# Kernel optimization log

Hardware: AMD Instinct MI355X
Metric: run time of the kernel (lower is better)

## Reference

```python
import jax, jax.numpy as jnp
import numpy as np

EMBED = 768
HEADS = 12
HEAD_DIM = EMBED // HEADS
HIDDEN = int(EMBED * 4.0)
EPS = 1e-5


def setup_inputs() -> dict:
    key = jax.random.key(0)
    ks = jax.random.split(key, 12)
    s = 0.02
    return {
        "x": jax.random.normal(ks[0], (8, 1024, EMBED), dtype=jnp.float32),
        # norm1 / norm2 (LayerNorm affine params)
        "g1": jnp.ones((EMBED,), jnp.float32),
        "b1": jnp.zeros((EMBED,), jnp.float32),
        "g2": jnp.ones((EMBED,), jnp.float32),
        "b2": jnp.zeros((EMBED,), jnp.float32),
        # attention weights (stored [in, out]; qkv_bias=False)
        "w_qkv": jax.random.normal(ks[1], (EMBED, 3 * EMBED), jnp.float32) * s,
        "w_proj": jax.random.normal(ks[2], (EMBED, EMBED), jnp.float32) * s,
        "b_proj": jnp.zeros((EMBED,), jnp.float32),
        # MLP weights
        "w_fc1": jax.random.normal(ks[3], (EMBED, HIDDEN), jnp.float32) * s,
        "b_fc1": jnp.zeros((HIDDEN,), jnp.float32),
        "w_fc2": jax.random.normal(ks[4], (HIDDEN, EMBED), jnp.float32) * s,
        "b_fc2": jnp.zeros((EMBED,), jnp.float32),
    }


def _layernorm(x, g, b):
    mu = jnp.mean(x, axis=-1, keepdims=True)
    var = jnp.var(x, axis=-1, keepdims=True)
    return (x - mu) * jax.lax.rsqrt(var + EPS) * g + b


def reference(x, g1, b1, g2, b2, w_qkv, w_proj, b_proj, w_fc1, b_fc1, w_fc2, b_fc2):
    B, N, C = x.shape
    scaling = HEAD_DIM ** (-0.5)

    # --- attention branch ---
    h = _layernorm(x, g1, b1)
    qkv = (h @ w_qkv).reshape(B, N, 3, HEADS, HEAD_DIM)
    q, k, v = qkv[:, :, 0], qkv[:, :, 1], qkv[:, :, 2]  # [B, N, H, D]
    attn = jnp.einsum("bnhd,bmhd->bhnm", q, k) * scaling  # full NxN scores
    attn = jax.nn.softmax(attn, axis=-1)
    out = jnp.einsum("bhnm,bmhd->bnhd", attn, v).reshape(B, N, C)
    out = out @ w_proj + b_proj
    x = x + out

    # --- MLP branch ---
    h = _layernorm(x, g2, b2)
    h = jax.nn.gelu(h @ w_fc1 + b_fc1, approximate=False)
    h = h @ w_fc2 + b_fc2
    return x + h
```

## Files before the change

kernel.cpp:

```cpp
#include <hip/hip_runtime.h>
#include <hip/hip_bf16.h>
#include <math.h>

#define EMBED 768
#define HEADS 12
#define HEAD_DIM 64
#define HIDDEN 3072
#define SEQ 1024
#define BATCH 8
#define TOKENS (SEQ*BATCH)

typedef unsigned short u16;
typedef __attribute__((ext_vector_type(8))) short bf16x8;
typedef __attribute__((ext_vector_type(4))) float floatx4;
typedef __attribute__((ext_vector_type(4))) u16 u16x4;
typedef __attribute__((ext_vector_type(2))) u16 u16x2;

__device__ __forceinline__ u16 f2bf(float f){
    union { float f; unsigned u; } v; v.f = f;
    unsigned r = v.u + 0x7fffu + ((v.u >> 16) & 1u);
    return (u16)(r >> 16);
}

__device__ __forceinline__ void gload16(const void* g, void* l){
    __builtin_amdgcn_global_load_lds((const __attribute__((address_space(1))) void*)g,
                                     (__attribute__((address_space(3))) void*)l, 16, 0, 0);
}

__device__ __forceinline__ float gelu_fast(float x){
    float t = 1.5957691216f * (x + 0.044715f * x * x * x);
    return x / (1.0f + __expf(-t));
}

__global__ void transpose_cast_all(const float* __restrict__ w0, const float* __restrict__ w1,
                                   const float* __restrict__ w2, const float* __restrict__ w3,
                                   u16* __restrict__ o0, u16* __restrict__ o1,
                                   u16* __restrict__ o2, u16* __restrict__ o3){
    int bb = blockIdx.x;
    const float* W; u16* Wt; int K, N, bx, by;
    if(bb < 1728)      { int l = bb;        W=w0; Wt=o0; K=768;  N=2304; bx=l%72; by=l/72; }
    else if(bb < 2304) { int l = bb-1728;   W=w1; Wt=o1; K=768;  N=768;  bx=l%24; by=l/24; }
    else if(bb < 4608) { int l = bb-2304;   W=w2; Wt=o2; K=768;  N=3072; bx=l%96; by=l/96; }
    else               { int l = bb-4608;   W=w3; Wt=o3; K=3072; N=768;  bx=l%24; by=l/24; }

    __shared__ float tile[32][33];
    int n0 = bx * 32, k0 = by * 32;
    int tx = threadIdx.x, ty = threadIdx.y;
    #pragma unroll
    for(int i=0;i<32;i+=8) tile[ty+i][tx] = W[(size_t)(k0+ty+i)*N + n0+tx];
    __syncthreads();
    int tid = ty*32 + tx;
    int kp = (tid & 15)*2, nn = tid >> 4;
    #pragma unroll
    for(int p=0;p<2;p++){
        int n = nn + p*16;
        u16x2 w2v;
        w2v.x = f2bf(tile[kp  ][n]);
        w2v.y = f2bf(tile[kp+1][n]);
        *(u16x2*)(Wt + (size_t)(n0+n)*K + k0 + kp) = w2v;
    }
}

__global__ __launch_bounds__(256) void ln_kernel(const float* __restrict__ x, const float* __restrict__ g,
                                                 const float* __restrict__ b, u16* __restrict__ out){
    int row  = blockIdx.x * 4 + (threadIdx.x >> 6);
    int lane = threadIdx.x & 63;
    const float4* xr = (const float4*)(x + (size_t)row * EMBED);
    float4 v[3];
    float s = 0.f;
    #pragma unroll
    for(int i=0;i<3;i++){
        v[i] = xr[i*64 + lane];
        s += v[i].x + v[i].y + v[i].z + v[i].w;
    }
    #pragma unroll
    for(int o=32;o>0;o>>=1) s += __shfl_xor(s, o);
    float mu = s * (1.0f/EMBED);
    float s2 = 0.f;
    #pragma unroll
    for(int i=0;i<3;i++){
        float dx = v[i].x-mu, dy = v[i].y-mu, dz = v[i].z-mu, dw = v[i].w-mu;
        s2 += dx*dx + dy*dy + dz*dz + dw*dw;
    }
    #pragma unroll
    for(int o=32;o>0;o>>=1) s2 += __shfl_xor(s2, o);
    float rstd = rsqrtf(s2*(1.0f/EMBED) + 1e-5f);
    u16* orow = out + (size_t)row * EMBED;
    const float4* g4 = (const float4*)g;
    const float4* b4 = (const float4*)b;
    #pragma unroll
    for(int i=0;i<3;i++){
        int c4 = i*64 + lane;
        float4 gv = g4[c4], bv = b4[c4];
        u16x4 pk;
        pk.x = f2bf((v[i].x-mu)*rstd*gv.x + bv.x);
        pk.y = f2bf((v[i].y-mu)*rstd*gv.y + bv.y);
        pk.z = f2bf((v[i].z-mu)*rstd*gv.z + bv.z);
        pk.w = f2bf((v[i].w-mu)*rstd*gv.w + bv.w);
        *(u16x4*)(orow + c4*4) = pk;
    }
}

template<int EPI, int BM>
__global__ __launch_bounds__(256) void gemm_bt(const u16* __restrict__ A, const u16* __restrict__ Bt,
        void* __restrict__ Cout, const float* __restrict__ bias, const float* __restrict__ res,
        u16* __restrict__ vt, int M, int N, int K, int ldc){
    constexpr int MF  = BM/32;
    constexpr int ASZ = BM*64;
    constexpr int BSZ = 128*64;
    __shared__ __align__(16) u16 As[2*ASZ];
    __shared__ __align__(16) u16 Bs[2*BSZ];
    int tid  = threadIdx.x;
    int wave = tid >> 6, lane = tid & 63;
    int quad = lane >> 4, lm = lane & 15;
    int m0 = blockIdx.y * BM, n0 = blockIdx.x * 128;
    int wm = (wave & 1) * (BM/2);
    int wn = (wave >> 1) * 64;

    floatx4 acc[MF][4];
    #pragma unroll
    for(int i=0;i<MF;i++)
        #pragma unroll
        for(int j=0;j<4;j++) acc[i][j] = (floatx4){0.f,0.f,0.f,0.f};

    int srow = tid >> 3;
    int scol = ((tid & 7) ^ (srow & 7)) * 8;
    const u16* aP[MF];
    const u16* bP[4];
    #pragma unroll
    for(int p=0;p<MF;p++) aP[p] = A  + (size_t)(m0 + p*32 + srow) * K + scol;
    #pragma unroll
    for(int p=0;p<4;p++)  bP[p] = Bt + (size_t)(n0 + p*32 + srow) * K + scol;

    #pragma unroll
    for(int p=0;p<MF;p++) gload16(aP[p], As + p*2048 + tid*8);
    #pragma unroll
    for(int p=0;p<4;p++)  gload16(bP[p], Bs + p*2048 + tid*8);
    __syncthreads();

    int cur = 0;
    for(int k0=0; k0<K; k0+=64){
        int nxt = cur ^ 1;
        if(k0 + 64 < K){
            #pragma unroll
            for(int p=0;p<MF;p++) gload16(aP[p] + k0 + 64, As + nxt*ASZ + p*2048 + tid*8);
            #pragma unroll
            for(int p=0;p<4;p++)  gload16(bP[p] + k0 + 64, Bs + nxt*BSZ + p*2048 + tid*8);
        }
        const u16* Asb = As + cur*ASZ;
        const u16* Bsb = Bs + cur*BSZ;
        #pragma unroll
        for(int ks=0;ks<2;ks++){
            int slotoff = (((ks*4+quad) ^ (lm&7)) << 3);
            bf16x8 af[MF], bfr[4];
            #pragma unroll
            for(int i=0;i<MF;i++)
                af[i]  = *(const bf16x8*)(Asb + (wm + i*16 + lm)*64 + slotoff);
            #pragma unroll
            for(int i=0;i<4;i++)
                bfr[i] = *(const bf16x8*)(Bsb + (wn + i*16 + lm)*64 + slotoff);
            #pragma unroll
            for(int mf=0;mf<MF;mf++)
                #pragma unroll
                for(int nf=0;nf<4;nf++)
                    acc[mf][nf] = __builtin_amdgcn_mfma_f32_16x16x32_bf16(af[mf], bfr[nf], acc[mf][nf], 0, 0, 0);
        }
        if(k0 + 64 < K) __syncthreads();
        cur = nxt;
    }

    if(EPI == 3 && n0 >= 1536){
        #pragma unroll
        for(int nf=0;nf<4;nf++){
            int col = n0 + wn + nf*16 + lm;
            int hh = (col - 1536) >> 6;
            int d  = col & 63;
            #pragma unroll
            for(int mf=0;mf<MF;mf++){
                int row0 = m0 + wm + mf*16 + quad*4;
                int bb  = row0 >> 10;
                int key = row0 & 1023;
                u16x4 pk;
                #pragma unroll
                for(int r=0;r<4;r++) pk[r] = f2bf(acc[mf][nf][r]);
                *(u16x4*)(vt + ((size_t)(bb*HEADS+hh)*64 + d)*SEQ + key) = pk;
            }
        }
        return;
    }

    #pragma unroll
    for(int nf=0;nf<4;nf++){
        int col = n0 + wn + nf*16 + lm;
        float bv = bias ? bias[col] : 0.f;
        #pragma unroll
        for(int mf=0;mf<MF;mf++){
            int row0 = m0 + wm + mf*16 + quad*4;
            #pragma unroll
            for(int r=0;r<4;r++){
                float v = acc[mf][nf][r] + bv;
                size_t idx = (size_t)(row0 + r) * ldc + col;
                if(EPI == 1){
                    v = gelu_fast(v);
                    ((u16*)Cout)[idx] = f2bf(v);
                } else if(EPI == 2){
                    ((float*)Cout)[idx] = v + res[idx];
                } else {
                    ((u16*)Cout)[idx] = f2bf(v);
                }
            }
        }
    }
}

__global__ __launch_bounds__(256) void attn_kernel(const u16* __restrict__ qk, const u16* __restrict__ vt,
                                                   u16* __restrict__ out){
    int qt = blockIdx.x, h = blockIdx.y, b = blockIdx.z;
    int tid = threadIdx.x;
    int wave = tid >> 6, lane = tid & 63;
    int quad = lane >> 4, lm = lane & 15;

    __shared__ __align__(16) u16 Ks[2*64*64];
    __shared__ __align__(16) u16 Vs[2*64*64];
    __shared__ __align__(16) u16 P[4*32*64];

    const u16* qbase = qk + (size_t)b * SEQ * 1536;
    const u16* vbase = vt + (size_t)(b*HEADS + h) * 64 * SEQ;
    u16* Pw = P + wave*2048;

    int q0 = qt*128 + wave*32;
    bf16x8 qf[2][2];
    #pragma unroll
    for(int qi=0;qi<2;qi++){
        const u16* qp = qbase + (size_t)(q0 + qi*16 + lm)*1536 + h*64;
        qf[qi][0] = *(const bf16x8*)(qp + quad*8);
        qf[qi][1] = *(const bf16x8*)(qp + 32 + quad*8);
    }

    float l_i[2] = {0.f, 0.f};
    floatx4 o_acc[2][4];
    #pragma unroll
    for(int qi=0;qi<2;qi++)
        #pragma unroll
        for(int nf=0;nf<4;nf++) o_acc[qi][nf] = (floatx4){0.f,0.f,0.f,0.f};

    int sr = lane >> 3;
    int sp = lane & 7;
    const float C = 0.18033688011112186f;

    auto stage = [&](int kt, int buf){
        #pragma unroll
        for(int i=0;i<2;i++){
            int rr = wave*16 + i*8 + sr;
            int sw = (sp ^ (rr & 7)) * 8;
            gload16(qbase + (size_t)(kt*64 + rr)*1536 + 768 + h*64 + sw,
                    Ks + buf*4096 + (wave*16 + i*8)*64 + lane*8);
            gload16(vbase + (size_t)rr*SEQ + kt*64 + sw,
                    Vs + buf*4096 + (wave*16 + i*8)*64 + lane*8);
        }
    };

    stage(0, 0);
    __syncthreads();

    int cur = 0;
    for(int kt=0; kt<16; kt++){
        if(kt < 15) stage(kt+1, cur^1);
        const u16* Ksb = Ks + cur*4096;
        const u16* Vsb = Vs + cur*4096;

        floatx4 s[4][2];
        #pragma unroll
        for(int kf=0;kf<4;kf++){
            int krow = kf*16 + lm;
            bf16x8 k0 = *(const bf16x8*)(Ksb + krow*64 + ((quad     ^ (lm&7))*8));
            bf16x8 k1 = *(const bf16x8*)(Ksb + krow*64 + (((4+quad) ^ (lm&7))*8));
            #pragma unroll
            for(int qi=0;qi<2;qi++){
                floatx4 t = (floatx4){0.f,0.f,0.f,0.f};
                t = __builtin_amdgcn_mfma_f32_16x16x32_bf16(k0, qf[qi][0], t, 0, 0, 0);
                t = __builtin_amdgcn_mfma_f32_16x16x32_bf16(k1, qf[qi][1], t, 0, 0, 0);
                s[kf][qi] = t;
            }
        }

        #pragma unroll
        for(int qi=0;qi<2;qi++){
            float part = 0.f;
            #pragma unroll
            for(int kf=0;kf<4;kf++){
                #pragma unroll
                for(int r=0;r<4;r++){
                    float e = exp2f(s[kf][qi][r]*C);
                    s[kf][qi][r] = e;
                    part += e;
                }
            }
            part += __shfl_xor(part, 16);
            part += __shfl_xor(part, 32);
            l_i[qi] += part;
            #pragma unroll
            for(int kf=0;kf<4;kf++){
                u16x4 pk;
                #pragma unroll
                for(int r=0;r<4;r++) pk[r] = f2bf(s[kf][qi][r]);
                int c  = kf*4 + quad;
                int cp = c ^ (2*(lm & 7));
                *(u16x4*)(Pw + (qi*16 + lm)*64 + cp*4) = pk;
            }
        }

        #pragma unroll
        for(int ks=0;ks<2;ks++){
            bf16x8 vf[4];
            #pragma unroll
            for(int nf=0;nf<4;nf++)
                vf[nf] = *(const bf16x8*)(Vsb + (nf*16+lm)*64 + (((ks*4+quad) ^ (lm&7))*8));
            #pragma unroll
            for(int qi=0;qi<2;qi++){
                int cr = (ks*8 + 2*quad) ^ (2*(lm & 7));
                bf16x8 pa = *(const bf16x8*)(Pw + (qi*16 + lm)*64 + cr*4);
                #pragma unroll
                for(int nf=0;nf<4;nf++)
                    o_acc[qi][nf] = __builtin_amdgcn_mfma_f32_16x16x32_bf16(pa, vf[nf], o_acc[qi][nf], 0, 0, 0);
            }
        }
        if(kt < 15) __syncthreads();
        cur ^= 1;
    }

    #pragma unroll
    for(int qi=0;qi<2;qi++){
        float rl[4];
        #pragma unroll
        for(int r=0;r<4;r++) rl[r] = 1.0f / __shfl(l_i[qi], quad*4 + r);
        int token = b*SEQ + qt*128 + wave*32 + qi*16 + quad*4;
        #pragma unroll
        for(int nf=0;nf<4;nf++){
            #pragma unroll
            for(int r=0;r<4;r++){
                out[(size_t)(token + r)*EMBED + h*64 + nf*16 + lm] = f2bf(o_acc[qi][nf][r] * rl[r]);
            }
        }
    }
}

extern "C" void kernel_launch(void* const* d_in, const int* in_sizes, int n_in,
                              void* d_out, int out_size, void* d_ws, size_t ws_size,
                              hipStream_t stream) {
    const float* x      = (const float*)d_in[0];
    const float* g1     = (const float*)d_in[1];
    const float* b1     = (const float*)d_in[2];
    const float* g2     = (const float*)d_in[3];
    const float* b2     = (const float*)d_in[4];
    const float* w_qkv  = (const float*)d_in[5];
    const float* w_proj = (const float*)d_in[6];
    const float* b_proj = (const float*)d_in[7];
    const float* w_fc1  = (const float*)d_in[8];
    const float* b_fc1  = (const float*)d_in[9];
    const float* w_fc2  = (const float*)d_in[10];
    const float* b_fc2  = (const float*)d_in[11];
    float* out = (float*)d_out;

    char* ws = (char*)d_ws;
    u16*   wqkv_t  = (u16*)  (ws + 0);
    u16*   wproj_t = (u16*)  (ws + 3538944);
    u16*   wfc1_t  = (u16*)  (ws + 4718592);
    u16*   wfc2_t  = (u16*)  (ws + 9437184);
    float* x1      = (float*)(ws + 14155776);
    u16*   hbuf    = (u16*)  (ws + 39321600);
    u16*   qkbuf   = (u16*)  (ws + 51904512);
    u16*   vtbuf   = (u16*)  (ws + 77070336);
    u16*   attn_o  = (u16*)  (ws + 89653248);
    u16*   fc1_o   = qkbuf;
    u16*   h2      = hbuf;

    transpose_cast_all<<<6912, dim3(32,8), 0, stream>>>(w_qkv, w_proj, w_fc1, w_fc2,
                                                        wqkv_t, wproj_t, wfc1_t, wfc2_t);

    ln_kernel<<<TOKENS/4, 256, 0, stream>>>(x, g1, b1, hbuf);

    gemm_bt<3,128><<<dim3(2304/128, TOKENS/128), 256, 0, stream>>>(hbuf, wqkv_t, qkbuf, nullptr, nullptr, vtbuf, TOKENS, 2304, 768, 1536);

    attn_kernel<<<dim3(8, HEADS, BATCH), 256, 0, stream>>>(qkbuf, vtbuf, attn_o);

    gemm_bt<2,64><<<dim3( 768/128, TOKENS/64), 256, 0, stream>>>(attn_o, wproj_t, x1, b_proj, x, nullptr, TOKENS, 768, 768, 768);

    ln_kernel<<<TOKENS/4, 256, 0, stream>>>(x1, g2, b2, h2);

    gemm_bt<1,128><<<dim3(3072/128, TOKENS/128), 256, 0, stream>>>(h2, wfc1_t, fc1_o, b_fc1, nullptr, nullptr, TOKENS, 3072, 768, 3072);

    gemm_bt<2,64><<<dim3( 768/128, TOKENS/64), 256, 0, stream>>>(fc1_o, wfc2_t, out, b_fc2, x1, nullptr, TOKENS, 768, 3072, 768);
}
```

Baseline: 381.2 us.

## Add wide 128x256 GEMM, single-buffer loads, swizzle blocks, fuse LN1 into prep

Adds a 512-thread GEMM kernel with 128x256 tiles for the QKV and FC1 projections, plus a grid swizzle across 8 groups meant to improve L2 locality. Both GEMM kernels drop LDS double-buffering for a single buffer with two barriers per k-step, which cuts shared memory use and may raise occupancy but exposes load latency. The first LayerNorm is folded into the weight transpose/cast kernel to remove one launch. Together these target launch overhead and GEMM tile reuse, at the risk of losing the overlap between global loads and MFMA.

```diff
diff --git a/kernel.cpp b/kernel.cpp
--- a/kernel.cpp
+++ b/kernel.cpp
@@ -32,11 +32,53 @@
     return x / (1.0f + __expf(-t));
 }
 
-__global__ void transpose_cast_all(const float* __restrict__ w0, const float* __restrict__ w1,
+__global__ __launch_bounds__(256) void prep_kernel(const float* __restrict__ w0, const float* __restrict__ w1,
                                    const float* __restrict__ w2, const float* __restrict__ w3,
                                    u16* __restrict__ o0, u16* __restrict__ o1,
-                                   u16* __restrict__ o2, u16* __restrict__ o3){
+                                   u16* __restrict__ o2, u16* __restrict__ o3,
+                                   const float* __restrict__ x, const float* __restrict__ g,
+                                   const float* __restrict__ bln, u16* __restrict__ lnout){
     int bb = blockIdx.x;
+    int tid = threadIdx.x;
+    if(bb >= 6912){
+        int row  = (bb - 6912) * 4 + (tid >> 6);
+        int lane = tid & 63;
+        const float4* xr = (const float4*)(x + (size_t)row * EMBED);
+        float4 v[3];
+        float s = 0.f;
+        #pragma unroll
+        for(int i=0;i<3;i++){
+            v[i] = xr[i*64 + lane];
+            s += v[i].x + v[i].y + v[i].z + v[i].w;
+        }
+        #pragma unroll
+        for(int o=32;o>0;o>>=1) s += __shfl_xor(s, o);
+        float mu = s * (1.0f/EMBED);
+        float s2 = 0.f;
+        #pragma unroll
+        for(int i=0;i<3;i++){
+            float dx = v[i].x-mu, dy = v[i].y-mu, dz = v[i].z-mu, dw = v[i].w-mu;
+            s2 += dx*dx + dy*dy + dz*dz + dw*dw;
+        }
+        #pragma unroll
+        for(int o=32;o>0;o>>=1) s2 += __shfl_xor(s2, o);
+        float rstd = rsqrtf(s2*(1.0f/EMBED) + 1e-5f);
+        u16* orow = lnout + (size_t)row * EMBED;
+        const float4* g4 = (const float4*)g;
+        const float4* b4 = (const float4*)bln;
+        #pragma unroll
+        for(int i=0;i<3;i++){
+            int c4 = i*64 + lane;
+            float4 gv = g4[c4], bv = b4[c4];
+            u16x4 pk;
+            pk.x = f2bf((v[i].x-mu)*rstd*gv.x + bv.x);
+            pk.y = f2bf((v[i].y-mu)*rstd*gv.y + bv.y);
+            pk.z = f2bf((v[i].z-mu)*rstd*gv.z + bv.z);
+            pk.w = f2bf((v[i].w-mu)*rstd*gv.w + bv.w);
+            *(u16x4*)(orow + c4*4) = pk;
+        }
+        return;
+    }
     const float* W; u16* Wt; int K, N, bx, by;
     if(bb < 1728)      { int l = bb;        W=w0; Wt=o0; K=768;  N=2304; bx=l%72; by=l/72; }
     else if(bb < 2304) { int l = bb-1728;   W=w1; Wt=o1; K=768;  N=768;  bx=l%24; by=l/24; }
@@ -45,11 +87,10 @@
 
     __shared__ float tile[32][33];
     int n0 = bx * 32, k0 = by * 32;
-    int tx = threadIdx.x, ty = threadIdx.y;
+    int tx = tid & 31, ty = tid >> 5;
     #pragma unroll
     for(int i=0;i<32;i+=8) tile[ty+i][tx] = W[(size_t)(k0+ty+i)*N + n0+tx];
     __syncthreads();
-    int tid = ty*32 + tx;
     int kp = (tid & 15)*2, nn = tid >> 4;
     #pragma unroll
     for(int p=0;p<2;p++){
@@ -101,72 +142,63 @@
     }
 }
 
-template<int EPI, int BM>
-__global__ __launch_bounds__(256) void gemm_bt(const u16* __restrict__ A, const u16* __restrict__ Bt,
+template<int EPI>
+__global__ __launch_bounds__(512,4) void gemm_wide(const u16* __restrict__ A, const u16* __restrict__ Bt,
         void* __restrict__ Cout, const float* __restrict__ bias, const float* __restrict__ res,
         u16* __restrict__ vt, int M, int N, int K, int ldc){
-    constexpr int MF  = BM/32;
-    constexpr int ASZ = BM*64;
-    constexpr int BSZ = 128*64;
-    __shared__ __align__(16) u16 As[2*ASZ];
-    __shared__ __align__(16) u16 Bs[2*BSZ];
+    __shared__ __align__(16) u16 As[128*64];
+    __shared__ __align__(16) u16 Bs[256*64];
     int tid  = threadIdx.x;
     int wave = tid >> 6, lane = tid & 63;
     int quad = lane >> 4, lm = lane & 15;
-    int m0 = blockIdx.y * BM, n0 = blockIdx.x * 128;
-    int wm = (wave & 1) * (BM/2);
-    int wn = (wave >> 1) * 64;
-
-    floatx4 acc[MF][4];
-    #pragma unroll
-    for(int i=0;i<MF;i++)
+    int wm = (wave >> 2) * 64;
+    int wn = (wave & 3) * 64;
+
+    int gx = gridDim.x;
+    int bid = blockIdx.y * gx + blockIdx.x;
+    int nwg = gx * gridDim.y;
+    int cpx = nwg >> 3;
+    int swz = (bid & 7) * cpx + (bid >> 3);
+    int m0 = (swz / gx) * 128, n0 = (swz % gx) * 256;
+
+    floatx4 acc[4][4];
+    #pragma unroll
+    for(int i=0;i<4;i++)
         #pragma unroll
         for(int j=0;j<4;j++) acc[i][j] = (floatx4){0.f,0.f,0.f,0.f};
 
     int srow = tid >> 3;
     int scol = ((tid & 7) ^ (srow & 7)) * 8;
-    const u16* aP[MF];
+    const u16* aP[2];
     const u16* bP[4];
     #pragma unroll
-    for(int p=0;p<MF;p++) aP[p] = A  + (size_t)(m0 + p*32 + srow) * K + scol;
-    #pragma unroll
-    for(int p=0;p<4;p++)  bP[p] = Bt + (size_t)(n0 + p*32 + srow) * K + scol;
-
-    #pragma unroll
-    for(int p=0;p<MF;p++) gload16(aP[p], As + p*2048 + tid*8);
-    #pragma unroll
-    for(int p=0;p<4;p++)  gload16(bP[p], Bs + p*2048 + tid*8);
-    __syncthreads();
-
-    int cur = 0;
+    for(int p=0;p<2;p++) aP[p] = A  + (size_t)(m0 + p*64 + srow) * K + scol;
+    #pragma unroll
+    for(int p=0;p<4;p++) bP[p] = Bt + (size_t)(n0 + p*64 + srow) * K + scol;
+
     for(int k0=0; k0<K; k0+=64){
-        int nxt = cur ^ 1;
-        if(k0 + 64 < K){
-            #pragma unroll
-            for(int p=0;p<MF;p++) gload16(aP[p] + k0 + 64, As + nxt*ASZ + p*2048 + tid*8);
-            #pragma unroll
-            for(int p=0;p<4;p++)  gload16(bP[p] + k0 + 64, Bs + nxt*BSZ + p*2048 + tid*8);
-        }
-        const u16* Asb = As + cur*ASZ;
-        const u16* Bsb = Bs + cur*BSZ;
+        __syncthreads();
+        #pragma unroll
+        for(int p=0;p<2;p++) gload16(aP[p] + k0, As + p*4096 + tid*8);
+        #pragma unroll
+        for(int p=0;p<4;p++) gload16(bP[p] + k0, Bs + p*4096 + tid*8);
+        __syncthreads();
         #pragma unroll
         for(int ks=0;ks<2;ks++){
             int slotoff = (((ks*4+quad) ^ (lm&7)) << 3);
-            bf16x8 af[MF], bfr[4];
-            #pragma unroll
-            for(int i=0;i<MF;i++)
-                af[i]  = *(const bf16x8*)(Asb + (wm + i*16 + lm)*64 + slotoff);
+            bf16x8 af[4], bfr[4];
             #pragma unroll
             for(int i=0;i<4;i++)
-                bfr[i] = *(const bf16x8*)(Bsb + (wn + i*16 + lm)*64 + slotoff);
-            #pragma unroll
-            for(int mf=0;mf<MF;mf++)
+                af[i]  = *(const bf16x8*)(As + (wm + i*16 + lm)*64 + slotoff);
+            #pragma unroll
+            for(int i=0;i<4;i++)
+                bfr[i] = *(const bf16x8*)(Bs + (wn + i*16 + lm)*64 + slotoff);
+            #pragma unroll
+            for(int mf=0;mf<4;mf++)
                 #pragma unroll
                 for(int nf=0;nf<4;nf++)
                     acc[mf][nf] = __builtin_amdgcn_mfma_f32_16x16x32_bf16(af[mf], bfr[nf], acc[mf][nf], 0, 0, 0);
         }
-        if(k0 + 64 < K) __syncthreads();
-        cur = nxt;
     }
 
     if(EPI == 3 && n0 >= 1536){
@@ -176,7 +208,7 @@
             int hh = (col - 1536) >> 6;
             int d  = col & 63;
             #pragma unroll
-            for(int mf=0;mf<MF;mf++){
+            for(int mf=0;mf<4;mf++){
                 int row0 = m0 + wm + mf*16 + quad*4;
                 int bb  = row0 >> 10;
                 int key = row0 & 1023;
@@ -194,7 +226,7 @@
         int col = n0 + wn + nf*16 + lm;
         float bv = bias ? bias[col] : 0.f;
         #pragma unroll
-        for(int mf=0;mf<MF;mf++){
+        for(int mf=0;mf<4;mf++){
             int row0 = m0 + wm + mf*16 + quad*4;
             #pragma unroll
             for(int r=0;r<4;r++){
@@ -203,7 +235,87 @@
                 if(EPI == 1){
                     v = gelu_fast(v);
                     ((u16*)Cout)[idx] = f2bf(v);
-                } else if(EPI == 2){
+                } else {
+                    ((u16*)Cout)[idx] = f2bf(v);
+                }
+            }
+        }
+    }
+}
+
+template<int EPI, int BM>
+__global__ __launch_bounds__(256) void gemm_bt(const u16* __restrict__ A, const u16* __restrict__ Bt,
+        void* __restrict__ Cout, const float* __restrict__ bias, const float* __restrict__ res,
+        u16* __restrict__ vt, int M, int N, int K, int ldc){
+    constexpr int MF = BM/32;
+    __shared__ __align__(16) u16 As[BM*64];
+    __shared__ __align__(16) u16 Bs[128*64];
+    int tid  = threadIdx.x;
+    int wave = tid >> 6, lane = tid & 63;
+    int quad = lane >> 4, lm = lane & 15;
+
+    int gx = gridDim.x;
+    int bid = blockIdx.y * gx + blockIdx.x;
+    int nwg = gx * gridDim.y;
+    int cpx = nwg >> 3;
+    int swz = (bid & 7) * cpx + (bid >> 3);
+    int m0 = (swz / gx) * BM, n0 = (swz % gx) * 128;
+
+    int wm = (wave & 1) * (BM/2);
+    int wn = (wave >> 1) * 64;
+
+    floatx4 acc[MF][4];
+    #pragma unroll
+    for(int i=0;i<MF;i++)
+        #pragma unroll
+        for(int j=0;j<4;j++) acc[i][j] = (floatx4){0.f,0.f,0.f,0.f};
+
+    int srow = tid >> 3;
+    int scol = ((tid & 7) ^ (srow & 7)) * 8;
+    const u16* aP[MF];
+    const u16* bP[4];
+    #pragma unroll
+    for(int p=0;p<MF;p++) aP[p] = A  + (size_t)(m0 + p*32 + srow) * K + scol;
+    #pragma unroll
+    for(int p=0;p<4;p++)  bP[p] = Bt + (size_t)(n0 + p*32 + srow) * K + scol;
+
+    for(int k0=0; k0<K; k0+=64){
+        __syncthreads();
+        #pragma unroll
+        for(int p=0;p<MF;p++) gload16(aP[p] + k0, As + p*2048 + tid*8);
+        #pragma unroll
+        for(int p=0;p<4;p++)  gload16(bP[p] + k0, Bs + p*2048 + tid*8);
+        __syncthreads();
+        #pragma unroll
+        for(int ks=0;ks<2;ks++){
+            int slotoff = (((ks*4+quad) ^ (lm&7)) << 3);
+            bf16x8 af[MF], bfr[4];
+            #pragma unroll
+            for(int i=0;i<MF;i++)
+                af[i]  = *(const bf16x8*)(As + (wm + i*16 + lm)*64 + slotoff);
+            #pragma unroll
+            for(int i=0;i<4;i++)
+                bfr[i] = *(const bf16x8*)(Bs + (wn + i*16 + lm)*64 + slotoff);
+            #pragma unroll
+            for(int mf=0;mf<MF;mf++)
+                #pragma unroll
+                for(int nf=0;nf<4;nf++)
+                    acc[mf][nf] = __builtin_amdgcn_mfma_f32_16x16x32_bf16(af[mf], bfr[nf], acc[mf][nf], 0, 0, 0);
+        }
+    }
+
+    #pragma unroll
+    for(int nf=0;nf<4;nf++){
+        int col = n0 + wn + nf*16 + lm;
+        float bv = bias ? bias[col] : 0.f;
+        #pragma unroll
+        for(int mf=0;mf<MF;mf++){
+            int row0 = m0 + wm + mf*16 + quad*4;
+            #pragma unroll
+            for(int r=0;r<4;r++){
+                float v = acc[mf][nf][r] + bv;
+                size_t idx = (size_t)(row0 + r) * ldc + col;
+                if(EPI == 2){
                     ((float*)Cout)[idx] = v + res[idx];
                 } else {
                     ((u16*)Cout)[idx] = f2bf(v);
@@ -375,12 +487,11 @@
     u16*   fc1_o   = qkbuf;
     u16*   h2      = hbuf;
 
-    transpose_cast_all<<<6912, dim3(32,8), 0, stream>>>(w_qkv, w_proj, w_fc1, w_fc2,
-                                                        wqkv_t, wproj_t, wfc1_t, wfc2_t);
-
-    ln_kernel<<<TOKENS/4, 256, 0, stream>>>(x, g1, b1, hbuf);
-
-    gemm_bt<3,128><<<dim3(2304/128, TOKENS/128), 256, 0, stream>>>(hbuf, wqkv_t, qkbuf, nullptr, nullptr, vtbuf, TOKENS, 2304, 768, 1536);
+    prep_kernel<<<8960, 256, 0, stream>>>(w_qkv, w_proj, w_fc1, w_fc2,
+                                          wqkv_t, wproj_t, wfc1_t, wfc2_t,
+                                          x, g1, b1, hbuf);
+
+    gemm_wide<3><<<dim3(2304/256, TOKENS/128), 512, 0, stream>>>(hbuf, wqkv_t, qkbuf, nullptr, nullptr, vtbuf, TOKENS, 2304, 768, 1536);
 
     attn_kernel<<<dim3(8, HEADS, BATCH), 256, 0, stream>>>(qkbuf, vtbuf, attn_o);
 
@@ -388,7 +499,7 @@
 
     ln_kernel<<<TOKENS/4, 256, 0, stream>>>(x1, g2, b2, h2);
 
-    gemm_bt<1,128><<<dim3(3072/128, TOKENS/128), 256, 0, stream>>>(h2, wfc1_t, fc1_o, b_fc1, nullptr, nullptr, TOKENS, 3072, 768, 3072);
+    gemm_wide<1><<<dim3(3072/256, TOKENS/128), 512, 0, stream>>>(h2, wfc1_t, fc1_o, b_fc1, nullptr, nullptr, TOKENS, 3072, 768, 3072);
 
     gemm_bt<2,64><<<dim3( 768/128, TOKENS/64), 256, 0, stream>>>(fc1_o, wfc2_t, out, b_fc2, x1, nullptr, TOKENS, 768, 3072, 768);
 }
```

Measured after the change: 348.9 us. 8.5% less time.
